# Kernel tuning notes

Measured on AMD Instinct MI355X. Metric: run time of the kernel, lower is better.

The kernel has to match this reference:

```python
import jax, jax.numpy as jnp
import numpy as np

B, S, HALF = 8, 2048, 512
D = 2 * HALF  # input_dim

def setup_inputs() -> dict:
    key = jax.random.key(0)
    ks = jax.random.split(key, 8)
    scale = 1.0 / np.sqrt(D)
    return {
        "t_out": jax.random.normal(ks[0], (B, S, HALF), dtype=jnp.float32),
        "c_out": jax.random.normal(ks[1], (B, S, HALF), dtype=jnp.float32),
        "Wq": jax.random.uniform(ks[2], (D, D), jnp.float32, -scale, scale),
        "bq": jax.random.uniform(ks[3], (D,), jnp.float32, -scale, scale),
        "Wk": jax.random.uniform(ks[4], (D, D), jnp.float32, -scale, scale),
        "bk": jax.random.uniform(ks[5], (D,), jnp.float32, -scale, scale),
        "Wv": jax.random.uniform(ks[6], (D, D), jnp.float32, -scale, scale),
        "bv": jax.random.uniform(ks[7], (D,), jnp.float32, -scale, scale),
    }

def reference(t_out, c_out, Wq, bq, Wk, bk, Wv, bv):
    # combined: [B, S, D]
    combined = jnp.concatenate([t_out, c_out], axis=-1)
    # torch nn.Linear: y = x @ W.T + b
    q = jnp.einsum('bsd,ed->bse', combined, Wq) + bq
    k = jnp.einsum('bsd,ed->bse', combined, Wk) + bk
    v = jnp.einsum('bsd,ed->bse', combined, Wv) + bv
    # Unscaled dot-product attention (no 1/sqrt(d) factor in original)
    scores = jnp.einsum('bqd,bkd->bqk', q, k)  # [B, S, S]
    attn = jax.nn.softmax(scores, axis=-1)
    return jnp.einsum('bqk,bkd->bqd', attn, v)
```

## Files before the change

### kernel.cpp

```cpp
#include <hip/hip_runtime.h>
#include <cstdint>
#include <cstddef>

typedef _Float16 f16;
typedef __attribute__((ext_vector_type(4))) _Float16 f16x4;
typedef __attribute__((ext_vector_type(8))) _Float16 f16x8;
typedef __attribute__((ext_vector_type(4))) float f32x4;

#define MFMA_F16(a, b, c) __builtin_amdgcn_mfma_f32_16x16x32_f16((a), (b), (c), 0, 0, 0)

static constexpr int BB   = 8;
static constexpr int SS   = 2048;
static constexpr int DD   = 1024;
static constexpr int HALF = 512;
static constexpr int T32  = 256 * 32;

__device__ __forceinline__ void gll16(const f16* g, f16* lds) {
  __builtin_amdgcn_global_load_lds(
      (__attribute__((address_space(1))) void*)(g),
      (__attribute__((address_space(3))) void*)(lds), 16, 0, 0);
}

__global__ __launch_bounds__(256) void fused_prep(
    const float* __restrict__ Wq, const float* __restrict__ Wk, const float* __restrict__ Wv,
    const float* __restrict__ t_out, const float* __restrict__ c_out,
    f16* __restrict__ Whq, f16* __restrict__ Whk, f16* __restrict__ Whv,
    f16* __restrict__ Xh)
{
  if (blockIdx.x < 1024) {
    const int i = (blockIdx.x * 256 + threadIdx.x) * 4;
    const float4 q = *(const float4*)(Wq + i);
    const float4 k = *(const float4*)(Wk + i);
    const float4 v = *(const float4*)(Wv + i);
    f16x4 a;
    a.x = (f16)q.x; a.y = (f16)q.y; a.z = (f16)q.z; a.w = (f16)q.w; *(f16x4*)(Whq + i) = a;
    a.x = (f16)k.x; a.y = (f16)k.y; a.z = (f16)k.z; a.w = (f16)k.w; *(f16x4*)(Whk + i) = a;
    a.x = (f16)v.x; a.y = (f16)v.y; a.z = (f16)v.z; a.w = (f16)v.w; *(f16x4*)(Whv + i) = a;
  } else {
    const size_t i = ((size_t)(blockIdx.x - 1024) * 256 + threadIdx.x) * 4;
    const int d = (int)(i & 1023);
    const size_t g = i >> 10;
    const float* src = (d < HALF) ? (t_out + g * HALF + d)
                                  : (c_out + g * HALF + (d - HALF));
    const float4 x = *(const float4*)src;
    f16x4 h;
    h.x = (f16)x.x; h.y = (f16)x.y; h.z = (f16)x.z; h.w = (f16)x.w;
    *(f16x4*)(Xh + i) = h;
  }
}

__device__ __forceinline__ void stage_half(
    f16* s, const f16* g, size_t r0, int ld, int k0, int u, int w4, int rr, int gg)
{
#pragma unroll
  for (int q = 0; q < 2; ++q) {
    const int rb  = u * 128 + w4 * 32 + q * 16;
    const int row = rb + rr;
    const int lg  = gg ^ ((row >> 1) & 3);
    gll16(g + (r0 + (size_t)row) * ld + k0 + lg * 8, s + (size_t)rb * 32);
  }
}

template <int K>
__device__ __forceinline__ void mma_pipeline(
    const f16* __restrict__ A, const f16* __restrict__ B,
    int lda, int ldb, size_t arow0, size_t brow0,
    f16* As, f16* Bs, f32x4 acc[8][4],
    int wave, int lane, int wm, int wn, int col16, int quad)
{
  constexpr int NT = K / 32;
  const int w4 = wave & 3, rr = lane >> 2, gg = lane & 3;
  const f16*  g_st  = (wave < 4) ? A : B;
  const size_t r0_st = (wave < 4) ? arow0 : brow0;
  const int    ld_st = (wave < 4) ? lda : ldb;
  f16*         ring  = (wave < 4) ? As : Bs;

#pragma unroll
  for (int pt = 0; pt < 3; ++pt)
#pragma unroll
    for (int u = 0; u < 2; ++u)
      stage_half(ring + pt * T32, g_st, r0_st, ld_st, pt * 32, u, w4, rr, gg);

  for (int t = 0; t < NT; ++t) {
    const f16* At = As + (t & 3) * T32;
    const f16* Bt = Bs + (t & 3) * T32;
    f16* Sn = ring + ((t + 3) & 3) * T32;
    const bool st = (t + 3 < NT);
    const int kn = (t + 3) * 32;

    f16x8 a[4], b[4];

    if (t < NT - 2)       asm volatile("s_waitcnt vmcnt(8)\n\ts_barrier" ::: "memory");
    else if (t == NT - 2) asm volatile("s_waitcnt vmcnt(4)\n\ts_barrier" ::: "memory");
    else                  asm volatile("s_waitcnt vmcnt(0)\n\ts_barrier" ::: "memory");
    if (st) stage_half(Sn, g_st, r0_st, ld_st, kn, 0, w4, rr, gg);
#pragma unroll
    for (int j = 0; j < 4; ++j) {
      const int r = wn * 64 + j * 16 + col16;
      b[j] = *(const f16x8*)&Bt[r * 32 + ((quad ^ ((r >> 1) & 3)) << 3)];
    }
#pragma unroll
    for (int i = 0; i < 4; ++i) {
      const int r = wm * 128 + i * 16 + col16;
      a[i] = *(const f16x8*)&At[r * 32 + ((quad ^ ((r >> 1) & 3)) << 3)];
    }
    __builtin_amdgcn_s_setprio(1);
#pragma unroll
    for (int i = 0; i < 4; ++i)
#pragma unroll
      for (int j = 0; j < 4; ++j)
        acc[i][j] = MFMA_F16(a[i], b[j], acc[i][j]);
    __builtin_amdgcn_s_setprio(0);

    if (t < NT - 2)       asm volatile("s_waitcnt vmcnt(8)\n\ts_barrier" ::: "memory");
    else if (t == NT - 2) asm volatile("s_waitcnt vmcnt(4)\n\ts_barrier" ::: "memory");
    else                  asm volatile("s_waitcnt vmcnt(0)\n\ts_barrier" ::: "memory");
    if (st) stage_half(Sn, g_st, r0_st, ld_st, kn, 1, w4, rr, gg);
#pragma unroll
    for (int i = 0; i < 4; ++i) {
      const int r = wm * 128 + 64 + i * 16 + col16;
      a[i] = *(const f16x8*)&At[r * 32 + ((quad ^ ((r >> 1) & 3)) << 3)];
    }
    __builtin_amdgcn_s_setprio(1);
#pragma unroll
    for (int i = 0; i < 4; ++i)
#pragma unroll
      for (int j = 0; j < 4; ++j)
        acc[i + 4][j] = MFMA_F16(a[i], b[j], acc[i + 4][j]);
    __builtin_amdgcn_s_setprio(0);
  }
}

__global__ __launch_bounds__(512, 2) void proj_gemm(
    const f16* __restrict__ Xh,
    const f16* __restrict__ Whq, const f16* __restrict__ Whk, const f16* __restrict__ Whv,
    const float* __restrict__ bq, const float* __restrict__ bk, const float* __restrict__ bv,
    f16* __restrict__ Q, f16* __restrict__ K, f16* __restrict__ Vv)
{
  __shared__ alignas(16) f16 As[4 * T32];
  __shared__ alignas(16) f16 Bs[4 * T32];

  const int z = blockIdx.z;
  const f16* Wh = (z == 0) ? Whq : (z == 1) ? Whk : Whv;
  const float* bias = (z == 0) ? bq : (z == 1) ? bk : bv;
  f16* dst = (z == 0) ? Q : (z == 1) ? K : Vv;

  const int t = threadIdx.x, lane = t & 63, wave = t >> 6;
  const int wm = wave >> 2, wn = wave & 3, col16 = lane & 15, quad = lane >> 4;
  const int m0 = blockIdx.x * 256, n0 = blockIdx.y * 256;

  f32x4 acc[8][4];
#pragma unroll
  for (int i = 0; i < 8; ++i)
#pragma unroll
    for (int j = 0; j < 4; ++j) acc[i][j] = f32x4{0.f, 0.f, 0.f, 0.f};

  mma_pipeline<DD>(Xh, Wh, DD, DD, (size_t)m0, (size_t)n0,
                   As, Bs, acc, wave, lane, wm, wn, col16, quad);

#pragma unroll
  for (int j = 0; j < 4; ++j) {
    const int gn = n0 + wn * 64 + j * 16 + col16;
    const float bb_ = bias[gn];
#pragma unroll
    for (int i = 0; i < 8; ++i) {
      const int gm = m0 + wm * 128 + i * 16 + quad * 4;
#pragma unroll
      for (int r = 0; r < 4; ++r)
        dst[(size_t)(gm + r) * DD + gn] = (f16)(acc[i][j][r] + bb_);
    }
  }
}

__global__ __launch_bounds__(256) void transpose_v(
    const f16* __restrict__ Vv, f16* __restrict__ Vt)
{
  __shared__ alignas(16) f16 tile[64][72];
  const int b  = blockIdx.z;
  const int s0 = blockIdx.x * 64;
  const int e0 = blockIdx.y * 64;
  const int t  = threadIdx.x;
  const int r  = t >> 3;
  const int c8 = (t & 7) * 8;

  const f16* src0 = Vv + ((size_t)(b * SS + s0 + r)) * DD + e0 + c8;
  const f16* src1 = Vv + ((size_t)(b * SS + s0 + r + 32)) * DD + e0 + c8;
  *(int4*)&tile[r][c8]      = *(const int4*)src0;
  *(int4*)&tile[r + 32][c8] = *(const int4*)src1;
  __syncthreads();

  f16x8 v0, v1;
#pragma unroll
  for (int u = 0; u < 8; ++u) {
    v0[u] = tile[c8 + u][r];
    v1[u] = tile[c8 + u][r + 32];
  }
  f16* dst0 = Vt + ((size_t)b * DD + e0 + r) * SS + s0 + c8;
  f16* dst1 = Vt + ((size_t)b * DD + e0 + r + 32) * SS + s0 + c8;
  *(f16x8*)dst0 = v0;
  *(f16x8*)dst1 = v1;
}

__global__ __launch_bounds__(512, 2) void qk_gemm(
    const f16* __restrict__ Q, const f16* __restrict__ K, f16* __restrict__ Sc,
    int b0)
{
  __shared__ alignas(16) f16 As[4 * T32];
  __shared__ alignas(16) f16 Bs[4 * T32];

  const int bb = blockIdx.z;
  const int t = threadIdx.x, lane = t & 63, wave = t >> 6;
  const int wm = wave >> 2, wn = wave & 3, col16 = lane & 15, quad = lane >> 4;
  const int m0 = blockIdx.y * 256, n0 = blockIdx.x * 256;

  const size_t arow0 = (size_t)(b0 + bb) * SS + m0;
  const size_t brow0 = (size_t)(b0 + bb) * SS + n0;

  f32x4 acc[8][4];
#pragma unroll
  for (int i = 0; i < 8; ++i)
#pragma unroll
    for (int j = 0; j < 4; ++j) acc[i][j] = f32x4{0.f, 0.f, 0.f, 0.f};

  mma_pipeline<DD>(Q, K, DD, DD, arow0, brow0,
                   As, Bs, acc, wave, lane, wm, wn, col16, quad);

#pragma unroll
  for (int i = 0; i < 8; ++i)
#pragma unroll
    for (int j = 0; j < 4; ++j)
#pragma unroll
      for (int r = 0; r < 4; ++r) {
        const int gm = m0 + wm * 128 + i * 16 + quad * 4 + r;
        const int gn = n0 + wn * 64 + j * 16 + col16;
        Sc[((size_t)bb * SS + gm) * SS + gn] = (f16)acc[i][j][r];
      }
}

__global__ __launch_bounds__(256) void softmax_rows(f16* __restrict__ Sc)
{
  const size_t row = blockIdx.x;
  f16* p = Sc + row * SS;
  const int t = threadIdx.x;

  const f16x8 v = *(const f16x8*)(p + t * 8);
  float xs[8];
#pragma unroll
  for (int u = 0; u < 8; ++u) xs[u] = (float)v[u];

  float m = xs[0];
#pragma unroll
  for (int u = 1; u < 8; ++u) m = fmaxf(m, xs[u]);
#pragma unroll
  for (int off = 32; off > 0; off >>= 1) m = fmaxf(m, __shfl_xor(m, off));
  __shared__ float redm[4];
  __shared__ float reds[4];
  if ((t & 63) == 0) redm[t >> 6] = m;
  __syncthreads();
  m = fmaxf(fmaxf(redm[0], redm[1]), fmaxf(redm[2], redm[3]));

  float e[8];
  float s = 0.f;
#pragma unroll
  for (int u = 0; u < 8; ++u) {
    e[u] = expf(xs[u] - m);
    s += e[u];
  }
#pragma unroll
  for (int off = 32; off > 0; off >>= 1) s += __shfl_xor(s, off);
  if ((t & 63) == 0) reds[t >> 6] = s;
  __syncthreads();
  s = reds[0] + reds[1] + reds[2] + reds[3];
  const float inv = 1.0f / s;

  f16x8 o;
#pragma unroll
  for (int u = 0; u < 8; ++u) o[u] = (f16)(e[u] * inv);
  *(f16x8*)(p + t * 8) = o;
}

__global__ __launch_bounds__(512, 2) void pv_gemm(
    const f16* __restrict__ P, const f16* __restrict__ Vt, float* __restrict__ out,
    int b0)
{
  __shared__ alignas(16) f16 As[4 * T32];
  __shared__ alignas(16) f16 Bs[4 * T32];

  const int bb = blockIdx.z;
  const int t = threadIdx.x, lane = t & 63, wave = t >> 6;
  const int wm = wave >> 2, wn = wave & 3, col16 = lane & 15, quad = lane >> 4;
  const int m0 = blockIdx.y * 256;
  const int n0 = blockIdx.x * 256;

  const size_t arow0 = (size_t)bb * SS + m0;
  const size_t brow0 = (size_t)(b0 + bb) * DD + n0;

  f32x4 acc[8][4];
#pragma unroll
  for (int i = 0; i < 8; ++i)
#pragma unroll
    for (int j = 0; j < 4; ++j) acc[i][j] = f32x4{0.f, 0.f, 0.f, 0.f};

  mma_pipeline<SS>(P, Vt, SS, SS, arow0, brow0,
                   As, Bs, acc, wave, lane, wm, wn, col16, quad);

#pragma unroll
  for (int i = 0; i < 8; ++i)
#pragma unroll
    for (int j = 0; j < 4; ++j)
#pragma unroll
      for (int r = 0; r < 4; ++r) {
        const int gm = m0 + wm * 128 + i * 16 + quad * 4 + r;
        const int gn = n0 + wn * 64 + j * 16 + col16;
        out[((size_t)(b0 + bb) * SS + gm) * DD + gn] = acc[i][j][r];
      }
}

extern "C" void kernel_launch(void* const* d_in, const int* in_sizes, int n_in,
                              void* d_out, int out_size, void* d_ws, size_t ws_size,
                              hipStream_t stream)
{
  const float* t_out = (const float*)d_in[0];
  const float* c_out = (const float*)d_in[1];
  const float* Wq    = (const float*)d_in[2];
  const float* bq    = (const float*)d_in[3];
  const float* Wk    = (const float*)d_in[4];
  const float* bk    = (const float*)d_in[5];
  const float* Wv    = (const float*)d_in[6];
  const float* bv    = (const float*)d_in[7];
  float* out = (float*)d_out;

  const size_t WELT  = (size_t)DD * DD;
  const size_t TD8   = (size_t)BB * SS * DD;
  const size_t XH_B  = TD8 * sizeof(f16);
  const size_t SC1_B = (size_t)SS * SS * sizeof(f16);

  const size_t FIXED = 3 * WELT * sizeof(f16) + 4 * XH_B;
  int c = 2;
  for (int cand : {8, 4}) {
    size_t xsc = (size_t)cand * SC1_B;
    if (xsc < XH_B) xsc = XH_B;
    if (FIXED + xsc <= ws_size) { c = cand; break; }
  }
  size_t xsc_bytes = (size_t)c * SC1_B;
  if (xsc_bytes < XH_B) xsc_bytes = XH_B;

  char* ws = (char*)d_ws;
  f16* Whq = (f16*)ws;
  f16* Whk = Whq + WELT;
  f16* Whv = Whk + WELT;
  char* XSc = (char*)(Whv + WELT);
  f16* Xh = (f16*)XSc;
  f16* Sc = (f16*)XSc;
  f16* Q  = (f16*)(XSc + xsc_bytes);
  f16* K  = Q  + TD8;
  f16* Vv = K  + TD8;
  f16* Vt = Vv + TD8;

  fused_prep<<<dim3(1024 + 16384), dim3(256), 0, stream>>>(
      Wq, Wk, Wv, t_out, c_out, Whq, Whk, Whv, Xh);
  proj_gemm<<<dim3(64, 4, 3), dim3(512), 0, stream>>>(
      Xh, Whq, Whk, Whv, bq, bk, bv, Q, K, Vv);
  transpose_v<<<dim3(32, 16, 8), dim3(256), 0, stream>>>(Vv, Vt);

  for (int b0 = 0; b0 < BB; b0 += c) {
    qk_gemm<<<dim3(8, 8, c), dim3(512), 0, stream>>>(Q, K, Sc, b0);
    softmax_rows<<<dim3(c * SS), dim3(256), 0, stream>>>(Sc);
    pv_gemm<<<dim3(4, 8, c), dim3(512), 0, stream>>>(Sc, Vt, out, b0);
  }
}
```

Baseline: 437.3 us.

## Restructure GEMM pipeline barriers and add XCD-aware block swizzle

Reorders the inner K-loop so LDS fragment reads are issued before the next async global-to-LDS stage, and waits on vmcnt and lgkmcnt separately with extra barriers around the MFMA clusters. A sched_barrier pins the instruction order. It also remaps linear block IDs so consecutive tiles land on the same XCD, aiming for better L2 reuse in the projection, QK and PV GEMMs. The added barriers can serialize waves and cost throughput, and the swizzle assumes the block count divides evenly by 8.

```diff
diff --git a/kernel.cpp b/kernel.cpp
--- a/kernel.cpp
+++ b/kernel.cpp
@@ -19,6 +19,20 @@
   __builtin_amdgcn_global_load_lds(
       (__attribute__((address_space(1))) void*)(g),
       (__attribute__((address_space(3))) void*)(lds), 16, 0, 0);
+}
+
+__device__ __forceinline__ dim3 xcd_swz() {
+  const int gx = gridDim.x, gy = gridDim.y;
+  const int lin = blockIdx.x + gx * (blockIdx.y + gy * blockIdx.z);
+  const int nwg = gx * gy * (int)gridDim.z;
+  const int q = nwg >> 3;
+  const int nlin = (lin & 7) * q + (lin >> 3);
+  dim3 r;
+  r.x = nlin % gx;
+  const int rest = nlin / gx;
+  r.y = rest % gy;
+  r.z = rest / gy;
+  return r;
 }
 
 __global__ __launch_bounds__(256) void fused_prep(
@@ -80,6 +94,8 @@
 #pragma unroll
     for (int u = 0; u < 2; ++u)
       stage_half(ring + pt * T32, g_st, r0_st, ld_st, pt * 32, u, w4, rr, gg);
+  asm volatile("s_waitcnt vmcnt(8)" ::: "memory");
+  __builtin_amdgcn_s_barrier();
 
   for (int t = 0; t < NT; ++t) {
     const f16* At = As + (t & 3) * T32;
@@ -90,10 +106,6 @@
 
     f16x8 a[4], b[4];
 
-    if (t < NT - 2)       asm volatile("s_waitcnt vmcnt(8)\n\ts_barrier" ::: "memory");
-    else if (t == NT - 2) asm volatile("s_waitcnt vmcnt(4)\n\ts_barrier" ::: "memory");
-    else                  asm volatile("s_waitcnt vmcnt(0)\n\ts_barrier" ::: "memory");
-    if (st) stage_half(Sn, g_st, r0_st, ld_st, kn, 0, w4, rr, gg);
 #pragma unroll
     for (int j = 0; j < 4; ++j) {
       const int r = wn * 64 + j * 16 + col16;
@@ -104,6 +116,13 @@
       const int r = wm * 128 + i * 16 + col16;
       a[i] = *(const f16x8*)&At[r * 32 + ((quad ^ ((r >> 1) & 3)) << 3)];
     }
+    if (st) stage_half(Sn, g_st, r0_st, ld_st, kn, 0, w4, rr, gg);
+    if (t < NT - 3)       asm volatile("s_waitcnt vmcnt(6)" ::: "memory");
+    else if (t == NT - 3) asm volatile("s_waitcnt vmcnt(4)" ::: "memory");
+    else                  asm volatile("s_waitcnt vmcnt(0)" ::: "memory");
+    __builtin_amdgcn_s_barrier();
+    asm volatile("s_waitcnt lgkmcnt(0)" ::: "memory");
+    __builtin_amdgcn_sched_barrier(0);
     __builtin_amdgcn_s_setprio(1);
 #pragma unroll
     for (int i = 0; i < 4; ++i)
@@ -111,16 +130,17 @@
       for (int j = 0; j < 4; ++j)
         acc[i][j] = MFMA_F16(a[i], b[j], acc[i][j]);
     __builtin_amdgcn_s_setprio(0);
-
-    if (t < NT - 2)       asm volatile("s_waitcnt vmcnt(8)\n\ts_barrier" ::: "memory");
-    else if (t == NT - 2) asm volatile("s_waitcnt vmcnt(4)\n\ts_barrier" ::: "memory");
-    else                  asm volatile("s_waitcnt vmcnt(0)\n\ts_barrier" ::: "memory");
-    if (st) stage_half(Sn, g_st, r0_st, ld_st, kn, 1, w4, rr, gg);
+    __builtin_amdgcn_s_barrier();
+
 #pragma unroll
     for (int i = 0; i < 4; ++i) {
       const int r = wm * 128 + 64 + i * 16 + col16;
       a[i] = *(const f16x8*)&At[r * 32 + ((quad ^ ((r >> 1) & 3)) << 3)];
     }
+    if (st) stage_half(Sn, g_st, r0_st, ld_st, kn, 1, w4, rr, gg);
+    __builtin_amdgcn_s_barrier();
+    asm volatile("s_waitcnt lgkmcnt(0)" ::: "memory");
+    __builtin_amdgcn_sched_barrier(0);
     __builtin_amdgcn_s_setprio(1);
 #pragma unroll
     for (int i = 0; i < 4; ++i)
@@ -128,6 +148,7 @@
       for (int j = 0; j < 4; ++j)
         acc[i + 4][j] = MFMA_F16(a[i], b[j], acc[i + 4][j]);
     __builtin_amdgcn_s_setprio(0);
+    __builtin_amdgcn_s_barrier();
   }
 }
 
@@ -140,14 +161,15 @@
   __shared__ alignas(16) f16 As[4 * T32];
   __shared__ alignas(16) f16 Bs[4 * T32];
 
-  const int z = blockIdx.z;
+  const dim3 bid = xcd_swz();
+  const int z = bid.z;
   const f16* Wh = (z == 0) ? Whq : (z == 1) ? Whk : Whv;
   const float* bias = (z == 0) ? bq : (z == 1) ? bk : bv;
   f16* dst = (z == 0) ? Q : (z == 1) ? K : Vv;
 
   const int t = threadIdx.x, lane = t & 63, wave = t >> 6;
   const int wm = wave >> 2, wn = wave & 3, col16 = lane & 15, quad = lane >> 4;
-  const int m0 = blockIdx.x * 256, n0 = blockIdx.y * 256;
+  const int m0 = bid.x * 256, n0 = bid.y * 256;
 
   f32x4 acc[8][4];
 #pragma unroll
@@ -208,10 +230,11 @@
   __shared__ alignas(16) f16 As[4 * T32];
   __shared__ alignas(16) f16 Bs[4 * T32];
 
-  const int bb = blockIdx.z;
+  const dim3 bid = xcd_swz();
+  const int bb = bid.z;
   const int t = threadIdx.x, lane = t & 63, wave = t >> 6;
   const int wm = wave >> 2, wn = wave & 3, col16 = lane & 15, quad = lane >> 4;
-  const int m0 = blockIdx.y * 256, n0 = blockIdx.x * 256;
+  const int m0 = bid.y * 256, n0 = bid.x * 256;
 
   const size_t arow0 = (size_t)(b0 + bb) * SS + m0;
   const size_t brow0 = (size_t)(b0 + bb) * SS + n0;
@@ -286,11 +309,12 @@
   __shared__ alignas(16) f16 As[4 * T32];
   __shared__ alignas(16) f16 Bs[4 * T32];
 
-  const int bb = blockIdx.z;
+  const dim3 bid = xcd_swz();
+  const int bb = bid.z;
   const int t = threadIdx.x, lane = t & 63, wave = t >> 6;
   const int wm = wave >> 2, wn = wave & 3, col16 = lane & 15, quad = lane >> 4;
-  const int m0 = blockIdx.y * 256;
-  const int n0 = blockIdx.x * 256;
+  const int m0 = bid.y * 256;
+  const int n0 = bid.x * 256;
 
   const size_t arow0 = (size_t)bb * SS + m0;
   const size_t brow0 = (size_t)(b0 + bb) * DD + n0;
```

Result: no change. 430.4 us (-1.6%).
